# Optimization experiments

Measured on AMD Instinct MI355X. Metric: run time of the kernel, lower is better.

## Reference

```python
import jax, jax.numpy as jnp
import numpy as np

EPS = 1e-5
N_NODES = 50000
DEG = 16
VOCAB = 1000


def _log0(x):
    # Poincare log map at the origin: artanh(||x||) * x/||x||
    n = jnp.linalg.norm(x, axis=-1, keepdims=True)
    n = jnp.clip(n, EPS, 1.0 - EPS)
    return jnp.arctanh(n) * x / n


def _exp0(v):
    # Poincare exp map at the origin: tanh(||v||) * v/||v||
    n = jnp.linalg.norm(v, axis=-1, keepdims=True)
    n = jnp.maximum(n, EPS)
    return jnp.tanh(n) * v / n


def _make_edges(key):
    # N*DEG random in-edges per graph + self loops (g_homo.add_edges(dst, dst))
    src = jax.random.randint(key, (N_NODES * DEG,), 0, N_NODES)
    dst = jnp.repeat(jnp.arange(N_NODES), DEG)
    loop = jnp.arange(N_NODES)
    return jnp.concatenate([src, loop]), jnp.concatenate([dst, loop])


def setup_inputs() -> dict:
    key = jax.random.key(0)
    ks = jax.random.split(key, 10)
    x = jax.random.randint(ks[0], (N_NODES, 3), 0, VOCAB)
    emb0 = jax.random.normal(ks[1], (VOCAB, 96), jnp.float32) * 0.05
    emb1 = jax.random.normal(ks[2], (VOCAB, 96), jnp.float32) * 0.05
    emb2 = jax.random.normal(ks[3], (VOCAB, 64), jnp.float32) * 0.05
    W_in = jax.random.normal(ks[4], (256, 256), jnp.float32) * 0.05
    b_in = jnp.zeros((256,), jnp.float32)
    W_out = jax.random.normal(ks[5], (256, 128), jnp.float32) * 0.05
    b_out = jnp.zeros((128,), jnp.float32)
    src0, dst0 = _make_edges(ks[6])
    src1, dst1 = _make_edges(ks[7])
    return {"x": x, "emb0": emb0, "emb1": emb1, "emb2": emb2,
            "W_in": W_in, "b_in": b_in, "W_out": W_out, "b_out": b_out,
            "src0": src0, "dst0": dst0, "src1": src1, "dst1": dst1}


def _hat_layer(h, src, dst):
    # reduce_func: exp0(mean_over_in_neighbors(log0(src_feat)))
    logh = _log0(h)                      # [N, D]
    msgs = logh[src]                     # gather per edge  [E, D]
    s = jax.ops.segment_sum(msgs, dst, num_segments=N_NODES)
    deg = jax.ops.segment_sum(jnp.ones((dst.shape[0], 1), h.dtype), dst,
                              num_segments=N_NODES)
    return _exp0(s / deg)


def reference(x, emb0, emb1, emb2, W_in, b_in, W_out, b_out,
              src0, dst0, src1, dst1):
    # SparseFeatureEncoder: per-feature embedding lookup, concat
    feat = jnp.concatenate([emb0[x[:, 0]], emb1[x[:, 1]], emb2[x[:, 2]]], axis=-1)
    # forward does x.clone().detach() before per-etype processing
    feat = jax.lax.stop_gradient(feat)
    h = _exp0(feat @ W_in + b_in)                       # fc_input + exp_map_zero
    h = _hat_layer(h, src0, dst0)
    h = jax.nn.relu(h)                                  # relu between layers
    h = _hat_layer(h, src1, dst1)
    h = _exp0(_log0(h) @ W_out + b_out)                 # final fc_output in tangent space
    return h
```

## Files before the change

### kernel.cpp

```cpp
#include <hip/hip_runtime.h>
#include <math.h>

#define N_NODES 50000
#define DEG 16
#define EPSF 1e-5f

typedef unsigned int uint;
typedef unsigned short ushort;
typedef unsigned char uchar;

using bf16x8 = __attribute__((ext_vector_type(8))) short;
using f32x4  = __attribute__((ext_vector_type(4))) float;

__device__ __forceinline__ uint f2bf_rn(float f) {
    uint u = __float_as_uint(f);
    return (u + 0x7FFFu + ((u >> 16) & 1u)) >> 16;
}
__device__ __forceinline__ uint pack2(float a, float b) {
    return f2bf_rn(a) | (f2bf_rn(b) << 16);
}

__device__ __forceinline__ float pl32_max(float v) {
#if __has_builtin(__builtin_amdgcn_permlane32_swap)
    auto r = __builtin_amdgcn_permlane32_swap((int)__float_as_uint(v), (int)__float_as_uint(v), false, false);
    return fmaxf(__uint_as_float((uint)r[0]), __uint_as_float((uint)r[1]));
#else
    return fmaxf(v, __shfl_xor(v, 32, 64));
#endif
}
__device__ __forceinline__ float pl16_max(float v) {
#if __has_builtin(__builtin_amdgcn_permlane16_swap)
    auto r = __builtin_amdgcn_permlane16_swap((int)__float_as_uint(v), (int)__float_as_uint(v), false, false);
    return fmaxf(__uint_as_float((uint)r[0]), __uint_as_float((uint)r[1]));
#else
    return fmaxf(v, __shfl_xor(v, 16, 64));
#endif
}
#define DPP_ROR_ADD(v, CTRL) \
    v += __uint_as_float((uint)__builtin_amdgcn_update_dpp(0, (int)__float_as_uint(v), (CTRL), 0xF, 0xF, false))
#define DPP_ROR_MAX(v, CTRL) \
    v = fmaxf(v, __uint_as_float((uint)__builtin_amdgcn_update_dpp(0, (int)__float_as_uint(v), (CTRL), 0xF, 0xF, false)))

__device__ __forceinline__ float red16_sum(float v) {
    DPP_ROR_ADD(v, 0x121); DPP_ROR_ADD(v, 0x122);
    DPP_ROR_ADD(v, 0x124); DPP_ROR_ADD(v, 0x128);
    return v;
}
__device__ __forceinline__ float red16_max(float v) {
    DPP_ROR_MAX(v, 0x121); DPP_ROR_MAX(v, 0x122);
    DPP_ROR_MAX(v, 0x124); DPP_ROR_MAX(v, 0x128);
    return v;
}

__device__ __forceinline__ float tanh_over_x(float nm) {
    float e = __expf(2.f * nm);
    float t = 1.f - __fdividef(2.f, e + 1.f);
    return __fdividef(t, nm);
}
__device__ __forceinline__ float atanh_over_x(float n) {
    float l = __logf(__fdividef(1.f + n, 1.f - n));
    return 0.5f * __fdividef(l, n);
}

__device__ __forceinline__ void acc4(float* acc, uint dw, float rs) {
    acc[0] = fmaf((float)(dw & 0xffu),         rs, acc[0]);
    acc[1] = fmaf((float)((dw >> 8) & 0xffu),  rs, acc[1]);
    acc[2] = fmaf((float)((dw >> 16) & 0xffu), rs, acc[2]);
    acc[3] = fmaf((float)(dw >> 24),           rs, acc[3]);
}

__global__ __launch_bounds__(256) void k_prep(
    const float* __restrict__ W_in, const float* __restrict__ W_out,
    const float* __restrict__ emb0, const float* __restrict__ emb1,
    const float* __restrict__ emb2,
    ushort* __restrict__ W_t, ushort* __restrict__ Wo_t,
    ushort* __restrict__ e0b, ushort* __restrict__ e1b, ushort* __restrict__ e2b)
{
    const int b = blockIdx.x, t = threadIdx.x;
    if (b < 256) {
        W_t[b * 256 + t] = (ushort)f2bf_rn(W_in[t * 256 + b]);
    } else if (b < 384) {
        const int n = b - 256;
        Wo_t[n * 256 + t] = (ushort)f2bf_rn(W_out[t * 128 + n]);
    } else {
        const int idx = (b - 384) * 256 + t;
        if (idx < 96000)        e0b[idx] = (ushort)f2bf_rn(emb0[idx]);
        else if (idx < 192000)  e1b[idx - 96000] = (ushort)f2bf_rn(emb1[idx - 96000]);
        else                    e2b[idx - 192000] = (ushort)f2bf_rn(emb2[idx - 192000]);
    }
}

__global__ __launch_bounds__(256) void k_projtab(
    const ushort* __restrict__ e0b, const ushort* __restrict__ e1b,
    const ushort* __restrict__ e2b, const ushort* __restrict__ W_t,
    float* __restrict__ P0, float* __restrict__ P1, float* __restrict__ P2)
{
    const int tbl = blockIdx.x / 63;
    const int mt  = blockIdx.x % 63;
    const int m0  = mt * 16;

    const ushort* eb = (tbl == 0) ? e0b : (tbl == 1) ? e1b : e2b;
    float* P         = (tbl == 0) ? P0  : (tbl == 1) ? P1  : P2;
    const int KS      = (tbl == 2) ? 2 : 3;
    const int kstride = (tbl == 2) ? 64 : 96;
    const int kofs    = tbl * 96;

    const int lane = threadIdx.x & 63;
    const int w    = threadIdx.x >> 6;
    const int l15  = lane & 15;
    const int lhi  = lane >> 4;

    f32x4 acc[4];
    #pragma unroll
    for (int nf = 0; nf < 4; ++nf) acc[nf] = (f32x4){0.f, 0.f, 0.f, 0.f};

    const int arow = min(m0 + l15, 999);
    const ushort* Ap = eb + (size_t)arow * kstride + lhi * 8;
    const ushort* Wp = W_t + (size_t)(w * 64 + l15) * 256 + kofs + lhi * 8;

    for (int kk = 0; kk < KS; ++kk) {
        bf16x8 f = *(const bf16x8*)(Ap + kk * 32);
        #pragma unroll
        for (int nf = 0; nf < 4; ++nf) {
            bf16x8 wv = *(const bf16x8*)(Wp + (size_t)nf * 16 * 256 + kk * 32);
            acc[nf] = __builtin_amdgcn_mfma_f32_16x16x32_bf16(wv, f, acc[nf], 0, 0, 0);
        }
    }

    const int m = m0 + l15;
    #pragma unroll
    for (int nf = 0; nf < 4; ++nf)
        *(float4*)&P[(size_t)m * 256 + w * 64 + nf * 16 + lhi * 4] =
            *(float4*)&acc[nf];
}

__global__ __launch_bounds__(256) void k_encode_gather(
    const int* __restrict__ x,
    const float* __restrict__ P0, const float* __restrict__ P1,
    const float* __restrict__ P2, const float* __restrict__ b_in,
    uchar* __restrict__ q1, float* __restrict__ rscale1)
{
    const int tid = threadIdx.x;
    const int gi  = tid >> 4;
    const int p   = tid & 15;
    const int v   = blockIdx.x * 16 + gi;

    const int x0 = x[v * 3 + 0];
    const int x1 = x[v * 3 + 1];
    const int x2 = x[v * 3 + 2];

    const float* p0 = P0 + (size_t)x0 * 256 + p * 16;
    const float* p1 = P1 + (size_t)x1 * 256 + p * 16;
    const float* p2 = P2 + (size_t)x2 * 256 + p * 16;
    const float* bp = b_in + p * 16;

    float tv[16];
    #pragma unroll
    for (int u = 0; u < 4; ++u) {
        float4 a = *(const float4*)(p0 + u * 4);
        float4 c = *(const float4*)(p1 + u * 4);
        float4 d = *(const float4*)(p2 + u * 4);
        float4 bb = *(const float4*)(bp + u * 4);
        tv[u * 4 + 0] = a.x + c.x + d.x + bb.x;
        tv[u * 4 + 1] = a.y + c.y + d.y + bb.y;
        tv[u * 4 + 2] = a.z + c.z + d.z + bb.z;
        tv[u * 4 + 3] = a.w + c.w + d.w + bb.w;
    }

    float lm = 0.f;
    #pragma unroll
    for (int i = 0; i < 16; ++i) lm = fmaxf(lm, fabsf(tv[i]));
    float rm = fmaxf(red16_max(lm), 1e-20f);
    const float qs = __fdividef(127.f, rm);

    uint d[4];
    #pragma unroll
    for (int k = 0; k < 4; ++k) {
        uint b0 = (uint)(int)rintf(fmaf(tv[4 * k + 0], qs, 128.f));
        uint b1 = (uint)(int)rintf(fmaf(tv[4 * k + 1], qs, 128.f));
        uint b2 = (uint)(int)rintf(fmaf(tv[4 * k + 2], qs, 128.f));
        uint b3 = (uint)(int)rintf(fmaf(tv[4 * k + 3], qs, 128.f));
        d[k] = b0 | (b1 << 8) | (b2 << 16) | (b3 << 24);
    }
    uint4 o; o.x = d[0]; o.y = d[1]; o.z = d[2]; o.w = d[3];
    *(uint4*)&q1[(size_t)v * 256 + p * 16] = o;
    if (p == 0) rscale1[v] = rm * (1.f / 127.f);
}

__global__ __launch_bounds__(256) void k_hat1_q(
    const uchar* __restrict__ q1, const float* __restrict__ rscale1,
    const int* __restrict__ src, ushort* __restrict__ l2)
{
    __shared__ int lsrc[256];
    const int tid = threadIdx.x;
    const int gi  = tid >> 4;
    const int p   = tid & 15;
    const int vb  = blockIdx.x * 16;
    const int v   = vb + gi;

    lsrc[tid] = src[(size_t)vb * DEG + tid];
    __syncthreads();

    float acc[16];
    #pragma unroll
    for (int i = 0; i < 16; i++) acc[i] = 0.f;
    float srs = 0.f;

    #pragma unroll 4
    for (int j = 0; j < DEG; ++j) {
        const int s = lsrc[(gi << 4) | j];
        uint4 r = *(const uint4*)(q1 + ((size_t)s << 8) + p * 16);
        float rs = rscale1[s];
        srs += rs;
        acc4(acc + 0, r.x, rs); acc4(acc + 4, r.y, rs);
        acc4(acc + 8, r.z, rs); acc4(acc + 12, r.w, rs);
    }
    {
        uint4 r = *(const uint4*)(q1 + ((size_t)v << 8) + p * 16);
        float rs = rscale1[v];
        srs += rs;
        acc4(acc + 0, r.x, rs); acc4(acc + 4, r.y, rs);
        acc4(acc + 8, r.z, rs); acc4(acc + 12, r.w, rs);
    }

    const float inv = 1.f / (float)(DEG + 1);
    const float bias = 128.f * srs;
    float rz[16], ss = 0.f, ssp = 0.f;
    #pragma unroll
    for (int i = 0; i < 16; i++) {
        float z = (acc[i] - bias) * inv;
        ss += z * z;
        rz[i] = fmaxf(z, 0.f);
        ssp += rz[i] * rz[i];
    }
    ss  = red16_sum(ss);
    ssp = red16_sum(ssp);

    float se = tanh_over_x(fmaxf(sqrtf(ss), EPSF));
    float nh = se * sqrtf(ssp);
    float nc = fminf(fmaxf(nh, EPSF), 1.f - EPSF);
    float c  = atanh_over_x(nc) * se;

    uint4 o1, o2;
    o1.x = pack2(c * rz[0],  c * rz[1]);
    o1.y = pack2(c * rz[2],  c * rz[3]);
    o1.z = pack2(c * rz[4],  c * rz[5]);
    o1.w = pack2(c * rz[6],  c * rz[7]);
    o2.x = pack2(c * rz[8],  c * rz[9]);
    o2.y = pack2(c * rz[10], c * rz[11]);
    o2.z = pack2(c * rz[12], c * rz[13]);
    o2.w = pack2(c * rz[14], c * rz[15]);
    ushort* row = l2 + (size_t)v * 256 + p * 16;
    *(uint4*)row = o1;
    *(uint4*)(row + 8) = o2;
}

__global__ __launch_bounds__(256) void k_fc_y(
    const ushort* __restrict__ l2, const ushort* __restrict__ Wo_t,
    const float* __restrict__ b_out,
    uchar* __restrict__ qy, float* __restrict__ rscale_y)
{
    const int t    = threadIdx.x;
    const int lane = t & 63;
    const int w    = t >> 6;
    const int l15  = lane & 15;
    const int lhi  = lane >> 4;
    const int m0   = blockIdx.x * 128;

    f32x4 acc[2][8];
    #pragma unroll
    for (int rf = 0; rf < 2; ++rf)
        #pragma unroll
        for (int nf = 0; nf < 8; ++nf)
            acc[rf][nf] = (f32x4){0.f, 0.f, 0.f, 0.f};

    const int ar0 = min(m0 + w * 32 + l15,      N_NODES - 1);
    const int ar1 = min(m0 + w * 32 + 16 + l15, N_NODES - 1);
    const ushort* Ap0 = l2 + (size_t)ar0 * 256 + lhi * 8;
    const ushort* Ap1 = l2 + (size_t)ar1 * 256 + lhi * 8;
    const ushort* Wp  = Wo_t + (size_t)l15 * 256 + lhi * 8;

    for (int kk = 0; kk < 8; ++kk) {
        bf16x8 f0 = *(const bf16x8*)(Ap0 + kk * 32);
        bf16x8 f1 = *(const bf16x8*)(Ap1 + kk * 32);
        #pragma unroll
        for (int nf = 0; nf < 8; ++nf) {
            bf16x8 wv = *(const bf16x8*)(Wp + (size_t)nf * 16 * 256 + kk * 32);
            acc[0][nf] = __builtin_amdgcn_mfma_f32_16x16x32_bf16(wv, f0, acc[0][nf], 0, 0, 0);
            acc[1][nf] = __builtin_amdgcn_mfma_f32_16x16x32_bf16(wv, f1, acc[1][nf], 0, 0, 0);
        }
    }

    float4 bb[8];
    #pragma unroll
    for (int nf = 0; nf < 8; ++nf)
        bb[nf] = *(const float4*)&b_out[nf * 16 + lhi * 4];

    #pragma unroll
    for (int rf = 0; rf < 2; ++rf) {
        const int m = m0 + w * 32 + rf * 16 + l15;
        float lm = 0.f;
        #pragma unroll
        for (int nf = 0; nf < 8; ++nf) {
            float t0 = acc[rf][nf][0] + bb[nf].x;
            float t1 = acc[rf][nf][1] + bb[nf].y;
            float t2 = acc[rf][nf][2] + bb[nf].z;
            float t3 = acc[rf][nf][3] + bb[nf].w;
            acc[rf][nf][0] = t0; acc[rf][nf][1] = t1;
            acc[rf][nf][2] = t2; acc[rf][nf][3] = t3;
            lm = fmaxf(lm, fmaxf(fmaxf(fabsf(t0), fabsf(t1)),
                                 fmaxf(fabsf(t2), fabsf(t3))));
        }
        lm = pl16_max(lm);
        lm = pl32_max(lm);
        lm = fmaxf(lm, 1e-20f);
        const float qs = __fdividef(127.f, lm);
        if (m < N_NODES) {
            #pragma unroll
            for (int nf = 0; nf < 8; ++nf) {
                uint b0 = (uint)(int)rintf(fmaf(acc[rf][nf][0], qs, 128.f));
                uint b1 = (uint)(int)rintf(fmaf(acc[rf][nf][1], qs, 128.f));
                uint b2 = (uint)(int)rintf(fmaf(acc[rf][nf][2], qs, 128.f));
                uint b3 = (uint)(int)rintf(fmaf(acc[rf][nf][3], qs, 128.f));
                *(uint*)&qy[(size_t)m * 128 + nf * 16 + lhi * 4] =
                    b0 | (b1 << 8) | (b2 << 16) | (b3 << 24);
            }
            if (lhi == 0) rscale_y[m] = lm * (1.f / 127.f);
        }
    }
}

__global__ __launch_bounds__(256) void k_hat2_q(
    const uchar* __restrict__ qy, const float* __restrict__ rscale_y,
    const int* __restrict__ src, float* __restrict__ out)
{
    __shared__ int lsrc[256];
    const int tid = threadIdx.x;
    const int gi  = tid >> 4;
    const int p   = tid & 15;
    const int vb  = blockIdx.x * 16;
    const int v   = vb + gi;

    lsrc[tid] = src[(size_t)vb * DEG + tid];
    __syncthreads();

    float acc[8];
    #pragma unroll
    for (int i = 0; i < 8; i++) acc[i] = 0.f;
    float srs = 0.f;

    #pragma unroll 4
    for (int j = 0; j < DEG; ++j) {
        const int s = lsrc[(gi << 4) | j];
        uint2 r = *(const uint2*)(qy + ((size_t)s << 7) + p * 8);
        float rs = rscale_y[s];
        srs += rs;
        acc4(acc + 0, r.x, rs); acc4(acc + 4, r.y, rs);
    }
    {
        uint2 r = *(const uint2*)(qy + ((size_t)v << 7) + p * 8);
        float rs = rscale_y[v];
        srs += rs;
        acc4(acc + 0, r.x, rs); acc4(acc + 4, r.y, rs);
    }

    const float inv = 1.f / (float)(DEG + 1);
    const float bias = 128.f * srs;
    float z[8], ss = 0.f;
    #pragma unroll
    for (int i = 0; i < 8; i++) {
        z[i] = (acc[i] - bias) * inv;
        ss += z[i] * z[i];
    }
    ss = red16_sum(ss);

    float se = tanh_over_x(fmaxf(sqrtf(ss), EPSF));

    float4 o0, o1;
    o0.x = se * z[0]; o0.y = se * z[1]; o0.z = se * z[2]; o0.w = se * z[3];
    o1.x = se * z[4]; o1.y = se * z[5]; o1.z = se * z[6]; o1.w = se * z[7];
    float* row = out + (size_t)v * 128 + p * 8;
    *(float4*)row = o0;
    *(float4*)(row + 4) = o1;
}

extern "C" void kernel_launch(void* const* d_in, const int* in_sizes, int n_in,
                              void* d_out, int out_size, void* d_ws, size_t ws_size,
                              hipStream_t stream) {
    const int*   x     = (const int*)  d_in[0];
    const float* emb0  = (const float*)d_in[1];
    const float* emb1  = (const float*)d_in[2];
    const float* emb2  = (const float*)d_in[3];
    const float* W_in  = (const float*)d_in[4];
    const float* b_in  = (const float*)d_in[5];
    const float* W_out = (const float*)d_in[6];
    const float* b_out = (const float*)d_in[7];
    const int*   src0  = (const int*)  d_in[8];
    const int*   src1  = (const int*)  d_in[10];
    float* out = (float*)d_out;

    uchar*  q1       = (uchar*)d_ws;
    ushort* l2       = (ushort*)(q1 + (size_t)N_NODES * 256);
    uchar*  qy       = (uchar*)(l2 + (size_t)N_NODES * 256);
    float*  rscale1  = (float*)(qy + (size_t)N_NODES * 128);
    float*  rscale_y = rscale1 + N_NODES;
    ushort* W_t      = (ushort*)(rscale_y + N_NODES);
    ushort* Wo_t     = W_t + 256 * 256;
    ushort* e0b      = Wo_t + 128 * 256;
    ushort* e1b      = e0b + 1000 * 96;
    ushort* e2b      = e1b + 1000 * 96;
    float*  P0       = (float*)(e2b + 1000 * 64);
    float*  P1       = P0 + 1024 * 256;
    float*  P2       = P1 + 1024 * 256;

    k_prep<<<1384, 256, 0, stream>>>(W_in, W_out, emb0, emb1, emb2,
                                     W_t, Wo_t, e0b, e1b, e2b);
    k_projtab<<<189, 256, 0, stream>>>(e0b, e1b, e2b, W_t, P0, P1, P2);
    k_encode_gather<<<N_NODES / 16, 256, 0, stream>>>(x, P0, P1, P2, b_in, q1, rscale1);
    k_hat1_q<<<N_NODES / 16, 256, 0, stream>>>(q1, rscale1, src0, l2);
    k_fc_y<<<(N_NODES + 127) / 128, 256, 0, stream>>>(l2, Wo_t, b_out, qy, rscale_y);
    k_hat2_q<<<N_NODES / 16, 256, 0, stream>>>(qy, rscale_y, src1, out);
}
```

Before: 100.7 us.

## Fuse hat layer 1 with output FC and fold embedding bf16 conversion into projtab

```diff
diff --git a/kernel.cpp b/kernel.cpp
--- a/kernel.cpp
+++ b/kernel.cpp
@@ -71,36 +71,28 @@
 
 __global__ __launch_bounds__(256) void k_prep(
     const float* __restrict__ W_in, const float* __restrict__ W_out,
-    const float* __restrict__ emb0, const float* __restrict__ emb1,
-    const float* __restrict__ emb2,
-    ushort* __restrict__ W_t, ushort* __restrict__ Wo_t,
-    ushort* __restrict__ e0b, ushort* __restrict__ e1b, ushort* __restrict__ e2b)
+    ushort* __restrict__ W_t, ushort* __restrict__ Wo_t)
 {
     const int b = blockIdx.x, t = threadIdx.x;
     if (b < 256) {
         W_t[b * 256 + t] = (ushort)f2bf_rn(W_in[t * 256 + b]);
-    } else if (b < 384) {
+    } else {
         const int n = b - 256;
         Wo_t[n * 256 + t] = (ushort)f2bf_rn(W_out[t * 128 + n]);
-    } else {
-        const int idx = (b - 384) * 256 + t;
-        if (idx < 96000)        e0b[idx] = (ushort)f2bf_rn(emb0[idx]);
-        else if (idx < 192000)  e1b[idx - 96000] = (ushort)f2bf_rn(emb1[idx - 96000]);
-        else                    e2b[idx - 192000] = (ushort)f2bf_rn(emb2[idx - 192000]);
     }
 }
 
 __global__ __launch_bounds__(256) void k_projtab(
-    const ushort* __restrict__ e0b, const ushort* __restrict__ e1b,
-    const ushort* __restrict__ e2b, const ushort* __restrict__ W_t,
+    const float* __restrict__ emb0, const float* __restrict__ emb1,
+    const float* __restrict__ emb2, const ushort* __restrict__ W_t,
     float* __restrict__ P0, float* __restrict__ P1, float* __restrict__ P2)
 {
     const int tbl = blockIdx.x / 63;
     const int mt  = blockIdx.x % 63;
     const int m0  = mt * 16;
 
-    const ushort* eb = (tbl == 0) ? e0b : (tbl == 1) ? e1b : e2b;
-    float* P         = (tbl == 0) ? P0  : (tbl == 1) ? P1  : P2;
+    const float* eb = (tbl == 0) ? emb0 : (tbl == 1) ? emb1 : emb2;
+    float* P        = (tbl == 0) ? P0   : (tbl == 1) ? P1   : P2;
     const int KS      = (tbl == 2) ? 2 : 3;
     const int kstride = (tbl == 2) ? 64 : 96;
     const int kofs    = tbl * 96;
@@ -115,11 +107,16 @@
     for (int nf = 0; nf < 4; ++nf) acc[nf] = (f32x4){0.f, 0.f, 0.f, 0.f};
 
     const int arow = min(m0 + l15, 999);
-    const ushort* Ap = eb + (size_t)arow * kstride + lhi * 8;
+    const float* Ap  = eb + (size_t)arow * kstride + lhi * 8;
     const ushort* Wp = W_t + (size_t)(w * 64 + l15) * 256 + kofs + lhi * 8;
 
     for (int kk = 0; kk < KS; ++kk) {
-        bf16x8 f = *(const bf16x8*)(Ap + kk * 32);
+        float4 v0 = *(const float4*)(Ap + kk * 32);
+        float4 v1 = *(const float4*)(Ap + kk * 32 + 4);
+        union { uint4 u; bf16x8 b; } cv;
+        cv.u.x = pack2(v0.x, v0.y); cv.u.y = pack2(v0.z, v0.w);
+        cv.u.z = pack2(v1.x, v1.y); cv.u.w = pack2(v1.z, v1.w);
+        bf16x8 f = cv.b;
         #pragma unroll
         for (int nf = 0; nf < 4; ++nf) {
             bf16x8 wv = *(const bf16x8*)(Wp + (size_t)nf * 16 * 256 + kk * 32);
@@ -187,11 +184,16 @@
     if (p == 0) rscale1[v] = rm * (1.f / 127.f);
 }
 
-__global__ __launch_bounds__(256) void k_hat1_q(
+__global__ __launch_bounds__(256) void k_hat1_fc(
     const uchar* __restrict__ q1, const float* __restrict__ rscale1,
-    const int* __restrict__ src, ushort* __restrict__ l2)
+    const int* __restrict__ src,
+    const ushort* __restrict__ Wo_t, const float* __restrict__ b_out,
+    uchar* __restrict__ qy, float* __restrict__ rscale_y)
 {
     __shared__ int lsrc[256];
+    __shared__ ushort T[16][264];
+    __shared__ float smaxq[4][16];
+
     const int tid = threadIdx.x;
     const int gi  = tid >> 4;
     const int p   = tid & 15;
@@ -250,84 +252,60 @@
     o2.y = pack2(c * rz[10], c * rz[11]);
     o2.z = pack2(c * rz[12], c * rz[13]);
     o2.w = pack2(c * rz[14], c * rz[15]);
-    ushort* row = l2 + (size_t)v * 256 + p * 16;
-    *(uint4*)row = o1;
-    *(uint4*)(row + 8) = o2;
-}
-
-__global__ __launch_bounds__(256) void k_fc_y(
-    const ushort* __restrict__ l2, const ushort* __restrict__ Wo_t,
-    const float* __restrict__ b_out,
-    uchar* __restrict__ qy, float* __restrict__ rscale_y)
-{
-    const int t    = threadIdx.x;
-    const int lane = t & 63;
-    const int w    = t >> 6;
+    *(uint4*)&T[gi][p * 16]     = o1;
+    *(uint4*)&T[gi][p * 16 + 8] = o2;
+    __syncthreads();
+
+    const int lane = tid & 63;
+    const int w    = tid >> 6;
     const int l15  = lane & 15;
     const int lhi  = lane >> 4;
-    const int m0   = blockIdx.x * 128;
-
-    f32x4 acc[2][8];
-    #pragma unroll
-    for (int rf = 0; rf < 2; ++rf)
+
+    f32x4 facc[2];
+    facc[0] = (f32x4){0.f, 0.f, 0.f, 0.f};
+    facc[1] = (f32x4){0.f, 0.f, 0.f, 0.f};
+
+    const ushort* Wp = Wo_t + (size_t)(w * 2 * 16 + l15) * 256 + lhi * 8;
+
+    for (int kk = 0; kk < 8; ++kk) {
+        bf16x8 f = *(const bf16x8*)&T[l15][kk * 32 + lhi * 8];
         #pragma unroll
-        for (int nf = 0; nf < 8; ++nf)
-            acc[rf][nf] = (f32x4){0.f, 0.f, 0.f, 0.f};
-
-    const int ar0 = min(m0 + w * 32 + l15,      N_NODES - 1);
-    const int ar1 = min(m0 + w * 32 + 16 + l15, N_NODES - 1);
-    const ushort* Ap0 = l2 + (size_t)ar0 * 256 + lhi * 8;
-    const ushort* Ap1 = l2 + (size_t)ar1 * 256 + lhi * 8;
-    const ushort* Wp  = Wo_t + (size_t)l15 * 256 + lhi * 8;
-
-    for (int kk = 0; kk < 8; ++kk) {
-        bf16x8 f0 = *(const bf16x8*)(Ap0 + kk * 32);
-        bf16x8 f1 = *(const bf16x8*)(Ap1 + kk * 32);
-        #pragma unroll
-        for (int nf = 0; nf < 8; ++nf) {
+        for (int nf = 0; nf < 2; ++nf) {
             bf16x8 wv = *(const bf16x8*)(Wp + (size_t)nf * 16 * 256 + kk * 32);
-            acc[0][nf] = __builtin_amdgcn_mfma_f32_16x16x32_bf16(wv, f0, acc[0][nf], 0, 0, 0);
-            acc[1][nf] = __builtin_amdgcn_mfma_f32_16x16x32_bf16(wv, f1, acc[1][nf], 0, 0, 0);
+            facc[nf] = __builtin_amdgcn_mfma_f32_16x16x32_bf16(wv, f, facc[nf], 0, 0, 0);
         }
     }
 
-    float4 bb[8];
-    #pragma unroll
-    for (int nf = 0; nf < 8; ++nf)
-        bb[nf] = *(const float4*)&b_out[nf * 16 + lhi * 4];
-
-    #pragma unroll
-    for (int rf = 0; rf < 2; ++rf) {
-        const int m = m0 + w * 32 + rf * 16 + l15;
-        float lm = 0.f;
-        #pragma unroll
-        for (int nf = 0; nf < 8; ++nf) {
-            float t0 = acc[rf][nf][0] + bb[nf].x;
-            float t1 = acc[rf][nf][1] + bb[nf].y;
-            float t2 = acc[rf][nf][2] + bb[nf].z;
-            float t3 = acc[rf][nf][3] + bb[nf].w;
-            acc[rf][nf][0] = t0; acc[rf][nf][1] = t1;
-            acc[rf][nf][2] = t2; acc[rf][nf][3] = t3;
-            lm = fmaxf(lm, fmaxf(fmaxf(fabsf(t0), fabsf(t1)),
-                                 fmaxf(fabsf(t2), fabsf(t3))));
-        }
-        lm = pl16_max(lm);
-        lm = pl32_max(lm);
-        lm = fmaxf(lm, 1e-20f);
-        const float qs = __fdividef(127.f, lm);
-        if (m < N_NODES) {
-            #pragma unroll
-            for (int nf = 0; nf < 8; ++nf) {
-                uint b0 = (uint)(int)rintf(fmaf(acc[rf][nf][0], qs, 128.f));
-                uint b1 = (uint)(int)rintf(fmaf(acc[rf][nf][1], qs, 128.f));
-                uint b2 = (uint)(int)rintf(fmaf(acc[rf][nf][2], qs, 128.f));
-                uint b3 = (uint)(int)rintf(fmaf(acc[rf][nf][3], qs, 128.f));
-                *(uint*)&qy[(size_t)m * 128 + nf * 16 + lhi * 4] =
-                    b0 | (b1 << 8) | (b2 << 16) | (b3 << 24);
-            }
-            if (lhi == 0) rscale_y[m] = lm * (1.f / 127.f);
-        }
-    }
+    float lm = 0.f;
+    #pragma unroll
+    for (int nf = 0; nf < 2; ++nf) {
+        float4 bb = *(const float4*)&b_out[(w * 2 + nf) * 16 + lhi * 4];
+        facc[nf][0] += bb.x; facc[nf][1] += bb.y;
+        facc[nf][2] += bb.z; facc[nf][3] += bb.w;
+        lm = fmaxf(lm, fmaxf(fmaxf(fabsf(facc[nf][0]), fabsf(facc[nf][1])),
+                             fmaxf(fabsf(facc[nf][2]), fabsf(facc[nf][3]))));
+    }
+    lm = pl16_max(lm);
+    lm = pl32_max(lm);
+    if (lhi == 0) smaxq[w][l15] = lm;
+    __syncthreads();
+
+    float rm = fmaxf(fmaxf(smaxq[0][l15], smaxq[1][l15]),
+                     fmaxf(smaxq[2][l15], smaxq[3][l15]));
+    rm = fmaxf(rm, 1e-20f);
+    const float qs = __fdividef(127.f, rm);
+    const int node = vb + l15;
+
+    #pragma unroll
+    for (int nf = 0; nf < 2; ++nf) {
+        uint b0 = (uint)(int)rintf(fmaf(facc[nf][0], qs, 128.f));
+        uint b1 = (uint)(int)rintf(fmaf(facc[nf][1], qs, 128.f));
+        uint b2 = (uint)(int)rintf(fmaf(facc[nf][2], qs, 128.f));
+        uint b3 = (uint)(int)rintf(fmaf(facc[nf][3], qs, 128.f));
+        *(uint*)&qy[(size_t)node * 128 + (w * 2 + nf) * 16 + lhi * 4] =
+            b0 | (b1 << 8) | (b2 << 16) | (b3 << 24);
+    }
+    if (tid < 16) rscale_y[vb + tid] = rm * (1.f / 127.f);
 }
 
 __global__ __launch_bounds__(256) void k_hat2_q(
@@ -400,24 +378,18 @@
     float* out = (float*)d_out;
 
     uchar*  q1       = (uchar*)d_ws;
-    ushort* l2       = (ushort*)(q1 + (size_t)N_NODES * 256);
-    uchar*  qy       = (uchar*)(l2 + (size_t)N_NODES * 256);
+    uchar*  qy       = q1 + (size_t)N_NODES * 256;
     float*  rscale1  = (float*)(qy + (size_t)N_NODES * 128);
     float*  rscale_y = rscale1 + N_NODES;
     ushort* W_t      = (ushort*)(rscale_y + N_NODES);
     ushort* Wo_t     = W_t + 256 * 256;
-    ushort* e0b      = Wo_t + 128 * 256;
-    ushort* e1b      = e0b + 1000 * 96;
-    ushort* e2b      = e1b + 1000 * 96;
-    float*  P0       = (float*)(e2b + 1000 * 64);
+    float*  P0       = (float*)(Wo_t + 128 * 256);
     float*  P1       = P0 + 1024 * 256;
     float*  P2       = P1 + 1024 * 256;
 
-    k_prep<<<1384, 256, 0, stream>>>(W_in, W_out, emb0, emb1, emb2,
-                                     W_t, Wo_t, e0b, e1b, e2b);
-    k_projtab<<<189, 256, 0, stream>>>(e0b, e1b, e2b, W_t, P0, P1, P2);
+    k_prep<<<384, 256, 0, stream>>>(W_in, W_out, W_t, Wo_t);
+    k_projtab<<<189, 256, 0, stream>>>(emb0, emb1, emb2, W_t, P0, P1, P2);
     k_encode_gather<<<N_NODES / 16, 256, 0, stream>>>(x, P0, P1, P2, b_in, q1, rscale1);
-    k_hat1_q<<<N_NODES / 16, 256, 0, stream>>>(q1, rscale1, src0, l2);
-    k_fc_y<<<(N_NODES + 127) / 128, 256, 0, stream>>>(l2, Wo_t, b_out, qy, rscale_y);
+    k_hat1_fc<<<N_NODES / 16, 256, 0, stream>>>(q1, rscale1, src0, Wo_t, b_out, qy, rscale_y);
     k_hat2_q<<<N_NODES / 16, 256, 0, stream>>>(qy, rscale_y, src1, out);
 }
```

After: 92.00 us. 1.09x faster.
